# Kernel tuning notes

Hardware: AMD Instinct MI355X
Metric: run time of the kernel (lower is better)

The kernel has to match this reference:

```python
import jax, jax.numpy as jnp
import numpy as np
import math

B, N, C, H, CH = 1, 256, 128, 4, 32  # batch, n_res, pair channels, heads, head dim
LN_EPS = 1e-5


def setup_inputs() -> dict:
    key = jax.random.key(0)
    ks = jax.random.split(key, 12)
    s = 0.02
    return {
        "act": jax.random.normal(ks[0], (B, N, N, C), dtype=jnp.float32),
        "mask": (jax.random.uniform(ks[1], (B, N, N)) < 0.9).astype(jnp.float32),
        "ln_g": jnp.ones((C,), jnp.float32),
        "ln_b": jnp.zeros((C,), jnp.float32),
        "wq": jax.random.normal(ks[2], (C, H * CH), jnp.float32) * s,
        "wk": jax.random.normal(ks[3], (C, H * CH), jnp.float32) * s,
        "wv": jax.random.normal(ks[4], (C, H * CH), jnp.float32) * s,
        "w2d": jax.random.normal(ks[5], (C, H), jnp.float32) * s,
        "wg": jax.random.normal(ks[6], (C, H * CH), jnp.float32) * s,
        "bg": jnp.ones((H * CH,), jnp.float32),
        "wo": jax.random.normal(ks[7], (H * CH, C), jnp.float32) * s,
        "bo": jnp.zeros((C,), jnp.float32),
    }


def reference(act, mask, ln_g, ln_b, wq, wk, wv, w2d, wg, bg, wo, bo):
    # swap the two residue axes: attend along the *starting* node axis
    x = jnp.swapaxes(act, -2, -3)          # [b, m, i, C]
    m = jnp.swapaxes(mask, -1, -2)         # [b, m, i]
    # LayerNorm
    mu = jnp.mean(x, axis=-1, keepdims=True)
    var = jnp.var(x, axis=-1, keepdims=True)
    x = (x - mu) * jax.lax.rsqrt(var + LN_EPS) * ln_g + ln_b
    # additive mask bias: [b, m, 1, 1, i]
    bias = (1e9 * (m - 1.0))[..., :, None, None, :]
    shp = x.shape[:-1]
    q = (x @ wq).reshape(*shp, H, CH)
    k = (x @ wk).reshape(*shp, H, CH)
    v = (x @ wv).reshape(*shp, H, CH)
    factor = 1.0 / math.sqrt(CH)
    aff = jnp.einsum('bmihc,bmjhc->bmhij', q * factor, k) + bias
    # non-batched pair bias: [b, h, m, i]; broadcasts against [b, m, h, i, j]
    # exactly as in the torch code (requires b == 1)
    nb = jnp.transpose(x @ w2d, (0, 3, 1, 2))
    weights = jax.nn.softmax(aff + nb, axis=-1)  # [b, m, h, i, j]
    g = jax.nn.sigmoid((x @ wg + bg).reshape(*shp, H, CH))
    out = jnp.einsum('bmhqk,bmkhc->bmqhc', weights, v) * g
    out = out.reshape(*shp, H * CH) @ wo + bo
    return jnp.swapaxes(out, -2, -3)
```

## Files before the change

### kernel.cpp

```cpp
#include <hip/hip_runtime.h>
#include <hip/hip_bf16.h>
#include <math.h>


typedef __attribute__((ext_vector_type(8))) short short8;
typedef __attribute__((ext_vector_type(4))) short short4v;
typedef __attribute__((ext_vector_type(4))) float f32x4;

__device__ __forceinline__ unsigned short f2bf(float f) {
  __hip_bfloat16 b = __float2bfloat16(f);
  return __builtin_bit_cast(unsigned short, b);
}
__device__ __forceinline__ float bf2f(unsigned short u) {
  return __uint_as_float(((unsigned int)u) << 16);
}

__device__ __forceinline__ f32x4 mfma16(short8 a, short8 b, f32x4 c) {
  return __builtin_amdgcn_mfma_f32_16x16x32_bf16(a, b, c, 0, 0, 0);
}

__global__ __launch_bounds__(256) void k_ln(const float* __restrict__ act,
                                            const float* __restrict__ ln_g,
                                            const float* __restrict__ ln_b,
                                            const float* __restrict__ wq,
                                            const float* __restrict__ wk,
                                            const float* __restrict__ wv,
                                            const float* __restrict__ wg,
                                            const float* __restrict__ w2d,
                                            const float* __restrict__ wo,
                                            const float* __restrict__ mask,
                                            unsigned short* __restrict__ lnxb,
                                            unsigned short* __restrict__ Wt4,
                                            unsigned short* __restrict__ Wto,
                                            float* __restrict__ maskT) {
  int t = threadIdx.x;
  if (blockIdx.x >= 4096) {
    int idx = (blockIdx.x - 4096) * 256 + t;
    if (idx < 65536) {
      int n = idx >> 7, k = idx & 127;
      const float* ws = (n < 128) ? wq : (n < 256) ? wk : (n < 384) ? wv : wg;
      Wt4[idx] = f2bf(ws[k * 128 + (n & 127)]);
    } else if (idx < 73728) {
      int j = idx - 65536;
      int r = j >> 7, k = j & 127;
      Wt4[idx] = (r < 4) ? f2bf(w2d[k * 4 + r]) : (unsigned short)0;
    } else if (idx < 90112) {
      int j = idx - 73728;
      int n = j >> 7, k = j & 127;
      Wto[j] = f2bf(wo[k * 128 + n]);
    } else if (idx < 155648) {
      int j2 = idx - 90112;
      int mi = j2 & 255, jj = j2 >> 8;
      maskT[mi * 256 + jj] = 1e9f * (mask[jj * 256 + mi] - 1.0f);
    }
    return;
  }
  int grp = t >> 4, l16 = t & 15;
  int row = blockIdx.x * 16 + grp;
  int mm = row >> 8, ii = row & 255;
  const float4* a = (const float4*)(act + ((size_t)(ii * 256 + mm)) * 128);
  float4 v0 = a[l16 * 2], v1 = a[l16 * 2 + 1];
  float s = (v0.x + v0.y) + (v0.z + v0.w) + (v1.x + v1.y) + (v1.z + v1.w);
  #pragma unroll
  for (int off = 1; off < 16; off <<= 1) s += __shfl_xor(s, off, 64);
  float mean = s * (1.f / 128.f);
  float e[8] = {v0.x - mean, v0.y - mean, v0.z - mean, v0.w - mean,
                v1.x - mean, v1.y - mean, v1.z - mean, v1.w - mean};
  float vs = (e[0]*e[0] + e[1]*e[1]) + (e[2]*e[2] + e[3]*e[3]) +
             (e[4]*e[4] + e[5]*e[5]) + (e[6]*e[6] + e[7]*e[7]);
  #pragma unroll
  for (int off = 1; off < 16; off <<= 1) vs += __shfl_xor(vs, off, 64);
  float rstd = rsqrtf(vs * (1.f / 128.f) + 1e-5f);
  const float4* gp = (const float4*)ln_g;
  const float4* bp = (const float4*)ln_b;
  float4 g0 = gp[l16 * 2], g1 = gp[l16 * 2 + 1];
  float4 b0 = bp[l16 * 2], b1 = bp[l16 * 2 + 1];
  short8 o;
  o[0] = (short)f2bf(e[0] * rstd * g0.x + b0.x);
  o[1] = (short)f2bf(e[1] * rstd * g0.y + b0.y);
  o[2] = (short)f2bf(e[2] * rstd * g0.z + b0.z);
  o[3] = (short)f2bf(e[3] * rstd * g0.w + b0.w);
  o[4] = (short)f2bf(e[4] * rstd * g1.x + b1.x);
  o[5] = (short)f2bf(e[5] * rstd * g1.y + b1.y);
  o[6] = (short)f2bf(e[6] * rstd * g1.z + b1.z);
  o[7] = (short)f2bf(e[7] * rstd * g1.w + b1.w);
  *(short8*)(lnxb + (size_t)row * 128 + l16 * 8) = o;
}

__global__ __launch_bounds__(256) void k_projg(const unsigned short* __restrict__ A,
                                               const unsigned short* __restrict__ Bt,
                                               const float* __restrict__ bg,
                                               unsigned short* __restrict__ qb,
                                               unsigned short* __restrict__ kb,
                                               unsigned short* __restrict__ vb,
                                               unsigned short* __restrict__ sgb,
                                               float* __restrict__ b2t) {
  __shared__ unsigned short As[128 * 40];
  __shared__ unsigned short Bs[64 * 40];
  int t = threadIdx.x;
  int m0 = blockIdx.x * 128, n0 = blockIdx.y * 64;
  int w = t >> 6, l = t & 63, g = l >> 4, li = l & 15;
  int wr = w >> 1, wc = w & 1;
  f32x4 acc[4][2] = {};
  for (int s = 0; s < 4; ++s) {
    int k0 = s * 32;
    __syncthreads();
    {
      int row = t >> 1, kl = (t & 1) * 16;
      const short8* src = (const short8*)(A + (size_t)(m0 + row) * 128 + k0 + kl);
      *(short8*)&As[row * 40 + kl]     = src[0];
      *(short8*)&As[row * 40 + kl + 8] = src[1];
      int bn = t >> 2, bk = (t & 3) * 8;
      *(short8*)&Bs[bn * 40 + bk] = *(const short8*)(Bt + (size_t)(n0 + bn) * 128 + k0 + bk);
    }
    __syncthreads();
    short8 af[4], bf[2];
    #pragma unroll
    for (int it = 0; it < 4; ++it)
      af[it] = *(const short8*)&As[(wr * 64 + it * 16 + li) * 40 + g * 8];
    #pragma unroll
    for (int jt = 0; jt < 2; ++jt)
      bf[jt] = *(const short8*)&Bs[(wc * 32 + jt * 16 + li) * 40 + g * 8];
    #pragma unroll
    for (int it = 0; it < 4; ++it)
      #pragma unroll
      for (int jt = 0; jt < 2; ++jt)
        acc[it][jt] = mfma16(bf[jt], af[it], acc[it][jt]);
  }
  int which = n0 >> 7;
  if (which == 4) {
    if (wc == 0 && g == 0) {
      #pragma unroll
      for (int it = 0; it < 4; ++it) {
        int R = m0 + wr * 64 + it * 16 + li;
        int mm = R >> 8, ii = R & 255;
        #pragma unroll
        for (int r = 0; r < 4; ++r)
          b2t[(size_t)r * 65536 + ii * 256 + mm] = acc[it][0][r];
      }
    }
    return;
  }
  const float factor = 0.17677669529663687f;
  #pragma unroll
  for (int it = 0; it < 4; ++it) {
    int R = m0 + wr * 64 + it * 16 + li;
    int mm = R >> 8, ii = R & 255;
    #pragma unroll
    for (int jt = 0; jt < 2; ++jt) {
      int nb4 = n0 + wc * 32 + jt * 16 + g * 4;
      int hh = (nb4 >> 5) & 3, ch = nb4 & 31;
      size_t o = ((size_t)((mm * 4 + hh) * 256 + ii)) * 32 + ch;
      short4v pk;
      if (which == 0) {
        #pragma unroll
        for (int r = 0; r < 4; ++r) pk[r] = (short)f2bf(acc[it][jt][r] * factor);
        *(short4v*)(qb + o) = pk;
      } else if (which == 1) {
        #pragma unroll
        for (int r = 0; r < 4; ++r) pk[r] = (short)f2bf(acc[it][jt][r]);
        *(short4v*)(kb + o) = pk;
      } else if (which == 2) {
        #pragma unroll
        for (int r = 0; r < 4; ++r) pk[r] = (short)f2bf(acc[it][jt][r]);
        *(short4v*)(vb + o) = pk;
      } else {
        #pragma unroll
        for (int r = 0; r < 4; ++r)
          pk[r] = (short)f2bf(1.f / (1.f + __expf(-(acc[it][jt][r] + bg[(nb4 & 127) + r]))));
        *(short4v*)(sgb + o) = pk;
      }
    }
  }
}

__global__ __launch_bounds__(256) void k_attn(const unsigned short* __restrict__ qb,
                                              const unsigned short* __restrict__ kb,
                                              const unsigned short* __restrict__ vb,
                                              const unsigned short* __restrict__ sgb,
                                              const float* __restrict__ b2t,
                                              const float* __restrict__ maskT,
                                              unsigned short* __restrict__ aob) {
  __shared__ unsigned short VT[32 * 264];
  __shared__ unsigned short Pl[4 * 32 * 72];
  __shared__ float maskls[256];
  int m = blockIdx.x >> 1, ihalf = blockIdx.x & 1, h = blockIdx.y;
  int t = threadIdx.x, w = t >> 6, l = t & 63, g = l >> 4, li = l & 15;
  int base = (m * 4 + h) << 8;
  maskls[t] = maskT[m * 256 + t];
  {
    const unsigned int* v32 = (const unsigned int*)(vb + (size_t)base * 32);
    #pragma unroll
    for (int p = 0; p < 16; ++p) {
      int idx = t + p * 256;
      int j = idx >> 4, cp = idx & 15;
      unsigned int u = v32[idx];
      VT[(cp * 2) * 264 + j]     = (unsigned short)(u & 0xffff);
      VT[(cp * 2 + 1) * 264 + j] = (unsigned short)(u >> 16);
    }
  }
  __syncthreads();
  int i0 = ihalf * 128 + w * 32;
  short8 qf[2];
  #pragma unroll
  for (int it = 0; it < 2; ++it)
    qf[it] = *(const short8*)(qb + ((size_t)(base + i0 + it * 16 + li)) * 32 + g * 8);
  float mst[2] = {-1e30f, -1e30f};
  float lst[2] = {0.f, 0.f};
  f32x4 oacc[2][2] = {};
  const float* b2 = b2t + (size_t)h * 65536;
  unsigned short* Pw = Pl + w * 32 * 72;
  for (int jc = 0; jc < 4; ++jc) {
    int j0 = jc * 64;
    f32x4 sacc[4][2];
    #pragma unroll
    for (int jt = 0; jt < 4; ++jt) {
      short8 kf = *(const short8*)(kb + ((size_t)(base + j0 + jt * 16 + li)) * 32 + g * 8);
      #pragma unroll
      for (int it = 0; it < 2; ++it) {
        f32x4 z = {0.f, 0.f, 0.f, 0.f};
        sacc[jt][it] = mfma16(kf, qf[it], z);
      }
    }
    #pragma unroll
    for (int it = 0; it < 2; ++it) {
      int ic = i0 + it * 16 + li;
      float s[16];
      float cmax = -1e30f;
      #pragma unroll
      for (int jt = 0; jt < 4; ++jt) {
        int jb = j0 + jt * 16 + g * 4;
        f32x4 mk = *(const f32x4*)&maskls[jb];
        #pragma unroll
        for (int r = 0; r < 4; ++r) {
          float sv = sacc[jt][it][r] + b2[(size_t)(jb + r) * 256 + ic] + mk[r];
          s[jt * 4 + r] = sv;
          cmax = fmaxf(cmax, sv);
        }
      }
      cmax = fmaxf(cmax, __shfl_xor(cmax, 16));
      cmax = fmaxf(cmax, __shfl_xor(cmax, 32));
      float mnew = fmaxf(mst[it], cmax);
      float fac = __expf(mst[it] - mnew);
      mst[it] = mnew;
      lst[it] *= fac;
      oacc[0][it] *= fac;
      oacc[1][it] *= fac;
      float psum = 0.f;
      #pragma unroll
      for (int jt = 0; jt < 4; ++jt) {
        float p0 = __expf(s[jt * 4 + 0] - mnew);
        float p1 = __expf(s[jt * 4 + 1] - mnew);
        float p2 = __expf(s[jt * 4 + 2] - mnew);
        float p3 = __expf(s[jt * 4 + 3] - mnew);
        psum += p0 + p1 + p2 + p3;
        short4v pk;
        pk.x = (short)f2bf(p0); pk.y = (short)f2bf(p1);
        pk.z = (short)f2bf(p2); pk.w = (short)f2bf(p3);
        *(short4v*)&Pw[(it * 16 + li) * 72 + jt * 16 + g * 4] = pk;
      }
      lst[it] += psum;
    }
    asm volatile("" ::: "memory");
    #pragma unroll
    for (int ks = 0; ks < 2; ++ks) {
      short8 vf0 = *(const short8*)&VT[li * 264        + j0 + ks * 32 + g * 8];
      short8 vf1 = *(const short8*)&VT[(16 + li) * 264 + j0 + ks * 32 + g * 8];
      #pragma unroll
      for (int it = 0; it < 2; ++it) {
        short8 pf = *(const short8*)&Pw[(it * 16 + li) * 72 + ks * 32 + g * 8];
        oacc[0][it] = mfma16(vf0, pf, oacc[0][it]);
        oacc[1][it] = mfma16(vf1, pf, oacc[1][it]);
      }
    }
    asm volatile("" ::: "memory");
  }
  #pragma unroll
  for (int it = 0; it < 2; ++it) {
    float lt = lst[it];
    lt += __shfl_xor(lt, 16);
    lt += __shfl_xor(lt, 32);
    float inv = 1.f / lt;
    int ic = i0 + it * 16 + li;
    #pragma unroll
    for (int ct = 0; ct < 2; ++ct) {
      int c0 = ct * 16 + g * 4;
      const unsigned short* grow = sgb + ((size_t)(base + ic)) * 32 + c0;
      ushort4 gu = *(const ushort4*)grow;
      ushort4 ov;
      ov.x = f2bf(oacc[ct][it][0] * inv * bf2f(gu.x));
      ov.y = f2bf(oacc[ct][it][1] * inv * bf2f(gu.y));
      ov.z = f2bf(oacc[ct][it][2] * inv * bf2f(gu.z));
      ov.w = f2bf(oacc[ct][it][3] * inv * bf2f(gu.w));
      *(ushort4*)&aob[((size_t)(ic * 256 + m)) * 128 + h * 32 + c0] = ov;
    }
  }
}

__global__ __launch_bounds__(256) void k_outg(const unsigned short* __restrict__ A,
                                              const unsigned short* __restrict__ Bt,
                                              const float* __restrict__ bo,
                                              float* __restrict__ out) {
  __shared__ unsigned short As[128 * 40];
  __shared__ unsigned short Bs[64 * 40];
  int t = threadIdx.x;
  int m0 = blockIdx.x * 128, n0 = blockIdx.y * 64;
  int w = t >> 6, l = t & 63, g = l >> 4, li = l & 15;
  int wr = w >> 1, wc = w & 1;
  f32x4 acc[4][2] = {};
  for (int s = 0; s < 4; ++s) {
    int k0 = s * 32;
    __syncthreads();
    {
      int row = t >> 1, kl = (t & 1) * 16;
      const short8* src = (const short8*)(A + (size_t)(m0 + row) * 128 + k0 + kl);
      *(short8*)&As[row * 40 + kl]     = src[0];
      *(short8*)&As[row * 40 + kl + 8] = src[1];
      int bn = t >> 2, bk = (t & 3) * 8;
      *(short8*)&Bs[bn * 40 + bk] = *(const short8*)(Bt + (size_t)(n0 + bn) * 128 + k0 + bk);
    }
    __syncthreads();
    short8 af[4], bf[2];
    #pragma unroll
    for (int it = 0; it < 4; ++it)
      af[it] = *(const short8*)&As[(wr * 64 + it * 16 + li) * 40 + g * 8];
    #pragma unroll
    for (int jt = 0; jt < 2; ++jt)
      bf[jt] = *(const short8*)&Bs[(wc * 32 + jt * 16 + li) * 40 + g * 8];
    #pragma unroll
    for (int it = 0; it < 4; ++it)
      #pragma unroll
      for (int jt = 0; jt < 2; ++jt)
        acc[it][jt] = mfma16(bf[jt], af[it], acc[it][jt]);
  }
  #pragma unroll
  for (int it = 0; it < 4; ++it) {
    int R = m0 + wr * 64 + it * 16 + li;
    #pragma unroll
    for (int jt = 0; jt < 2; ++jt) {
      int nb4 = n0 + wc * 32 + jt * 16 + g * 4;
      float4 o;
      o.x = acc[it][jt][0] + bo[nb4 + 0];
      o.y = acc[it][jt][1] + bo[nb4 + 1];
      o.z = acc[it][jt][2] + bo[nb4 + 2];
      o.w = acc[it][jt][3] + bo[nb4 + 3];
      *(float4*)(out + (size_t)R * 128 + nb4) = o;
    }
  }
}

extern "C" void kernel_launch(void* const* d_in, const int* in_sizes, int n_in,
                              void* d_out, int out_size, void* d_ws, size_t ws_size,
                              hipStream_t stream) {
  const float* act  = (const float*)d_in[0];
  const float* mask = (const float*)d_in[1];
  const float* ln_g = (const float*)d_in[2];
  const float* ln_b = (const float*)d_in[3];
  const float* wq   = (const float*)d_in[4];
  const float* wk   = (const float*)d_in[5];
  const float* wv   = (const float*)d_in[6];
  const float* w2d  = (const float*)d_in[7];
  const float* wg   = (const float*)d_in[8];
  const float* bg   = (const float*)d_in[9];
  const float* wo   = (const float*)d_in[10];
  const float* bo   = (const float*)d_in[11];

  char* p = (char*)d_ws;
  unsigned short* lnxb  = (unsigned short*)p;  p += (size_t)8388608 * 2;
  float*          b2t   = (float*)p;           p += (size_t)262144 * 4;
  unsigned short* qb    = (unsigned short*)p;  p += (size_t)8388608 * 2;
  unsigned short* kb    = (unsigned short*)p;  p += (size_t)8388608 * 2;
  unsigned short* vb    = (unsigned short*)p;  p += (size_t)8388608 * 2;
  unsigned short* sgb   = (unsigned short*)p;  p += (size_t)8388608 * 2;
  unsigned short* aob   = (unsigned short*)p;  p += (size_t)8388608 * 2;
  unsigned short* Wt4   = (unsigned short*)p;  p += (size_t)73728 * 2;
  unsigned short* Wto   = (unsigned short*)p;  p += (size_t)16384 * 2;
  float*          maskT = (float*)p;           p += (size_t)65536 * 4;
  float* out = (float*)d_out;

  hipLaunchKernelGGL(k_ln,    dim3(4704),     dim3(256), 0, stream,
                     act, ln_g, ln_b, wq, wk, wv, wg, w2d, wo, mask, lnxb, Wt4, Wto, maskT);
  hipLaunchKernelGGL(k_projg, dim3(512, 9),   dim3(256), 0, stream, lnxb, Wt4, bg, qb, kb, vb, sgb, b2t);
  hipLaunchKernelGGL(k_attn,  dim3(512, 4),   dim3(256), 0, stream, qb, kb, vb, sgb, b2t, maskT, aob);
  hipLaunchKernelGGL(k_outg,  dim3(512, 2),   dim3(256), 0, stream, aob, Wto, bo, out);
}
```

Baseline: 95.72 us.

## Stage full A row tile once in LDS and loop over all output columns

The projection and output GEMMs now load each 128x128 bf16 A tile into shared memory once per block and loop over every N block inside the kernel, instead of launching one block per (M,N) tile. This removes the repeated A reloads from global memory and the per-K-step barriers. Weight fragments are now read straight from global memory, relying on cache. The grid shrinks to 512 blocks, which lowers parallelism and occupancy and serialises the N work within each block.

```diff
diff --git a/kernel.cpp b/kernel.cpp
--- a/kernel.cpp
+++ b/kernel.cpp
@@ -95,80 +95,81 @@
                                                unsigned short* __restrict__ vb,
                                                unsigned short* __restrict__ sgb,
                                                float* __restrict__ b2t) {
-  __shared__ unsigned short As[128 * 40];
-  __shared__ unsigned short Bs[64 * 40];
+  __shared__ unsigned short As[128 * 136];
   int t = threadIdx.x;
-  int m0 = blockIdx.x * 128, n0 = blockIdx.y * 64;
+  int m0 = blockIdx.x * 128;
   int w = t >> 6, l = t & 63, g = l >> 4, li = l & 15;
   int wr = w >> 1, wc = w & 1;
-  f32x4 acc[4][2] = {};
-  for (int s = 0; s < 4; ++s) {
-    int k0 = s * 32;
-    __syncthreads();
-    {
-      int row = t >> 1, kl = (t & 1) * 16;
-      const short8* src = (const short8*)(A + (size_t)(m0 + row) * 128 + k0 + kl);
-      *(short8*)&As[row * 40 + kl]     = src[0];
-      *(short8*)&As[row * 40 + kl + 8] = src[1];
-      int bn = t >> 2, bk = (t & 3) * 8;
-      *(short8*)&Bs[bn * 40 + bk] = *(const short8*)(Bt + (size_t)(n0 + bn) * 128 + k0 + bk);
-    }
-    __syncthreads();
-    short8 af[4], bf[2];
-    #pragma unroll
-    for (int it = 0; it < 4; ++it)
-      af[it] = *(const short8*)&As[(wr * 64 + it * 16 + li) * 40 + g * 8];
-    #pragma unroll
-    for (int jt = 0; jt < 2; ++jt)
-      bf[jt] = *(const short8*)&Bs[(wc * 32 + jt * 16 + li) * 40 + g * 8];
-    #pragma unroll
-    for (int it = 0; it < 4; ++it)
+  {
+    int row = t >> 1, c0 = (t & 1) * 64;
+    const unsigned short* src = A + (size_t)(m0 + row) * 128 + c0;
+    #pragma unroll
+    for (int k8 = 0; k8 < 8; ++k8)
+      *(short8*)&As[row * 136 + c0 + k8 * 8] = *(const short8*)(src + k8 * 8);
+  }
+  __syncthreads();
+  const float factor = 0.17677669529663687f;
+  for (int nb = 0; nb < 9; ++nb) {
+    int n0 = nb * 64;
+    f32x4 acc[4][2] = {};
+    #pragma unroll
+    for (int s = 0; s < 4; ++s) {
+      int k0 = s * 32;
+      short8 af[4], bf[2];
+      #pragma unroll
+      for (int it = 0; it < 4; ++it)
+        af[it] = *(const short8*)&As[(wr * 64 + it * 16 + li) * 136 + k0 + g * 8];
       #pragma unroll
       for (int jt = 0; jt < 2; ++jt)
-        acc[it][jt] = mfma16(bf[jt], af[it], acc[it][jt]);
-  }
-  int which = n0 >> 7;
-  if (which == 4) {
-    if (wc == 0 && g == 0) {
-      #pragma unroll
-      for (int it = 0; it < 4; ++it) {
-        int R = m0 + wr * 64 + it * 16 + li;
-        int mm = R >> 8, ii = R & 255;
+        bf[jt] = *(const short8*)(Bt + (size_t)(n0 + wc * 32 + jt * 16 + li) * 128 + k0 + g * 8);
+      #pragma unroll
+      for (int it = 0; it < 4; ++it)
         #pragma unroll
-        for (int r = 0; r < 4; ++r)
-          b2t[(size_t)r * 65536 + ii * 256 + mm] = acc[it][0][r];
-      }
-    }
-    return;
-  }
-  const float factor = 0.17677669529663687f;
-  #pragma unroll
-  for (int it = 0; it < 4; ++it) {
-    int R = m0 + wr * 64 + it * 16 + li;
-    int mm = R >> 8, ii = R & 255;
-    #pragma unroll
-    for (int jt = 0; jt < 2; ++jt) {
-      int nb4 = n0 + wc * 32 + jt * 16 + g * 4;
-      int hh = (nb4 >> 5) & 3, ch = nb4 & 31;
-      size_t o = ((size_t)((mm * 4 + hh) * 256 + ii)) * 32 + ch;
-      short4v pk;
-      if (which == 0) {
+        for (int jt = 0; jt < 2; ++jt)
+          acc[it][jt] = mfma16(bf[jt], af[it], acc[it][jt]);
+    }
+    int which = n0 >> 7;
+    if (which == 4) {
+      if (wc == 0 && g == 0) {
         #pragma unroll
-        for (int r = 0; r < 4; ++r) pk[r] = (short)f2bf(acc[it][jt][r] * factor);
-        *(short4v*)(qb + o) = pk;
-      } else if (which == 1) {
-        #pragma unroll
-        for (int r = 0; r < 4; ++r) pk[r] = (short)f2bf(acc[it][jt][r]);
-        *(short4v*)(kb + o) = pk;
-      } else if (which == 2) {
-        #pragma unroll
-        for (int r = 0; r < 4; ++r) pk[r] = (short)f2bf(acc[it][jt][r]);
-        *(short4v*)(vb + o) = pk;
-      } else {
-        #pragma unroll
-        for (int r = 0; r < 4; ++r)
-          pk[r] = (short)f2bf(1.f / (1.f + __expf(-(acc[it][jt][r] + bg[(nb4 & 127) + r]))));
-        *(short4v*)(sgb + o) = pk;
+        for (int it = 0; it < 4; ++it) {
+          int R = m0 + wr * 64 + it * 16 + li;
+          int mm = R >> 8, ii = R & 255;
+          #pragma unroll
+          for (int r = 0; r < 4; ++r)
+            b2t[(size_t)r * 65536 + ii * 256 + mm] = acc[it][0][r];
+        }
+      }
+      continue;
+    }
+    #pragma unroll
+    for (int it = 0; it < 4; ++it) {
+      int R = m0 + wr * 64 + it * 16 + li;
+      int mm = R >> 8, ii = R & 255;
+      #pragma unroll
+      for (int jt = 0; jt < 2; ++jt) {
+        int nb4 = n0 + wc * 32 + jt * 16 + g * 4;
+        int hh = (nb4 >> 5) & 3, ch = nb4 & 31;
+        size_t o = ((size_t)((mm * 4 + hh) * 256 + ii)) * 32 + ch;
+        short4v pk;
+        if (which == 0) {
+          #pragma unroll
+          for (int r = 0; r < 4; ++r) pk[r] = (short)f2bf(acc[it][jt][r] * factor);
+          *(short4v*)(qb + o) = pk;
+        } else if (which == 1) {
+          #pragma unroll
+          for (int r = 0; r < 4; ++r) pk[r] = (short)f2bf(acc[it][jt][r]);
+          *(short4v*)(kb + o) = pk;
+        } else if (which == 2) {
+          #pragma unroll
+          for (int r = 0; r < 4; ++r) pk[r] = (short)f2bf(acc[it][jt][r]);
+          *(short4v*)(vb + o) = pk;
+        } else {
+          #pragma unroll
+          for (int r = 0; r < 4; ++r)
+            pk[r] = (short)f2bf(1.f / (1.f + __expf(-(acc[it][jt][r] + bg[(nb4 & 127) + r]))));
+          *(short4v*)(sgb + o) = pk;
+        }
       }
     }
   }
@@ -301,50 +302,52 @@
                                               const unsigned short* __restrict__ Bt,
                                               const float* __restrict__ bo,
                                               float* __restrict__ out) {
-  __shared__ unsigned short As[128 * 40];
-  __shared__ unsigned short Bs[64 * 40];
+  __shared__ unsigned short As[128 * 136];
   int t = threadIdx.x;
-  int m0 = blockIdx.x * 128, n0 = blockIdx.y * 64;
+  int m0 = blockIdx.x * 128;
   int w = t >> 6, l = t & 63, g = l >> 4, li = l & 15;
   int wr = w >> 1, wc = w & 1;
-  f32x4 acc[4][2] = {};
-  for (int s = 0; s < 4; ++s) {
-    int k0 = s * 32;
-    __syncthreads();
-    {
-      int row = t >> 1, kl = (t & 1) * 16;
-      const short8* src = (const short8*)(A + (size_t)(m0 + row) * 128 + k0 + kl);
-      *(short8*)&As[row * 40 + kl]     = src[0];
-      *(short8*)&As[row * 40 + kl + 8] = src[1];
-      int bn = t >> 2, bk = (t & 3) * 8;
-      *(short8*)&Bs[bn * 40 + bk] = *(const short8*)(Bt + (size_t)(n0 + bn) * 128 + k0 + bk);
-    }
-    __syncthreads();
-    short8 af[4], bf[2];
-    #pragma unroll
-    for (int it = 0; it < 4; ++it)
-      af[it] = *(const short8*)&As[(wr * 64 + it * 16 + li) * 40 + g * 8];
-    #pragma unroll
-    for (int jt = 0; jt < 2; ++jt)
-      bf[jt] = *(const short8*)&Bs[(wc * 32 + jt * 16 + li) * 40 + g * 8];
-    #pragma unroll
-    for (int it = 0; it < 4; ++it)
+  {
+    int row = t >> 1, c0 = (t & 1) * 64;
+    const unsigned short* src = A + (size_t)(m0 + row) * 128 + c0;
+    #pragma unroll
+    for (int k8 = 0; k8 < 8; ++k8)
+      *(short8*)&As[row * 136 + c0 + k8 * 8] = *(const short8*)(src + k8 * 8);
+  }
+  __syncthreads();
+  #pragma unroll
+  for (int nb = 0; nb < 2; ++nb) {
+    int n0 = nb * 64;
+    f32x4 acc[4][2] = {};
+    #pragma unroll
+    for (int s = 0; s < 4; ++s) {
+      int k0 = s * 32;
+      short8 af[4], bf[2];
+      #pragma unroll
+      for (int it = 0; it < 4; ++it)
+        af[it] = *(const short8*)&As[(wr * 64 + it * 16 + li) * 136 + k0 + g * 8];
       #pragma unroll
       for (int jt = 0; jt < 2; ++jt)
-        acc[it][jt] = mfma16(bf[jt], af[it], acc[it][jt]);
-  }
-  #pragma unroll
-  for (int it = 0; it < 4; ++it) {
-    int R = m0 + wr * 64 + it * 16 + li;
-    #pragma unroll
-    for (int jt = 0; jt < 2; ++jt) {
-      int nb4 = n0 + wc * 32 + jt * 16 + g * 4;
-      float4 o;
-      o.x = acc[it][jt][0] + bo[nb4 + 0];
-      o.y = acc[it][jt][1] + bo[nb4 + 1];
-      o.z = acc[it][jt][2] + bo[nb4 + 2];
-      o.w = acc[it][jt][3] + bo[nb4 + 3];
-      *(float4*)(out + (size_t)R * 128 + nb4) = o;
+        bf[jt] = *(const short8*)(Bt + (size_t)(n0 + wc * 32 + jt * 16 + li) * 128 + k0 + g * 8);
+      #pragma unroll
+      for (int it = 0; it < 4; ++it)
+        #pragma unroll
+        for (int jt = 0; jt < 2; ++jt)
+          acc[it][jt] = mfma16(bf[jt], af[it], acc[it][jt]);
+    }
+    #pragma unroll
+    for (int it = 0; it < 4; ++it) {
+      int R = m0 + wr * 64 + it * 16 + li;
+      #pragma unroll
+      for (int jt = 0; jt < 2; ++jt) {
+        int nb4 = n0 + wc * 32 + jt * 16 + g * 4;
+        float4 o;
+        o.x = acc[it][jt][0] + bo[nb4 + 0];
+        o.y = acc[it][jt][1] + bo[nb4 + 1];
+        o.z = acc[it][jt][2] + bo[nb4 + 2];
+        o.w = acc[it][jt][3] + bo[nb4 + 3];
+        *(float4*)(out + (size_t)R * 128 + nb4) = o;
+      }
     }
   }
 }
@@ -378,9 +381,9 @@
   float*          maskT = (float*)p;           p += (size_t)65536 * 4;
   float* out = (float*)d_out;
 
-  hipLaunchKernelGGL(k_ln,    dim3(4704),     dim3(256), 0, stream,
+  hipLaunchKernelGGL(k_ln,    dim3(4704),   dim3(256), 0, stream,
                      act, ln_g, ln_b, wq, wk, wv, wg, w2d, wo, mask, lnxb, Wt4, Wto, maskT);
-  hipLaunchKernelGGL(k_projg, dim3(512, 9),   dim3(256), 0, stream, lnxb, Wt4, bg, qb, kb, vb, sgb, b2t);
-  hipLaunchKernelGGL(k_attn,  dim3(512, 4),   dim3(256), 0, stream, qb, kb, vb, sgb, b2t, maskT, aob);
-  hipLaunchKernelGGL(k_outg,  dim3(512, 2),   dim3(256), 0, stream, aob, Wto, bo, out);
-}
+  hipLaunchKernelGGL(k_projg, dim3(512),    dim3(256), 0, stream, lnxb, Wt4, bg, qb, kb, vb, sgb, b2t);
+  hipLaunchKernelGGL(k_attn,  dim3(512, 4), dim3(256), 0, stream, qb, kb, vb, sgb, b2t, maskT, aob);
+  hipLaunchKernelGGL(k_outg,  dim3(512),    dim3(256), 0, stream, aob, Wto, bo, out);
+}
```

Result: slower. 104.0 us (+8.7%).
